# Kernel optimization log

Hardware: AMD Instinct MI355X
Metric: run time of the kernel (lower is better)

## Reference

```python
import jax, jax.numpy as jnp
import numpy as np

N, B, C, H = 1024, 4, 256, 8
D = C // H


def _make_boxes(k):
    u = jax.random.uniform(k, (N, 4), dtype=jnp.float32)
    x1 = u[:, 0] * 500.0
    y1 = u[:, 1] * 500.0
    x2 = x1 + u[:, 2] * 200.0 + 1.0
    y2 = y1 + u[:, 3] * 200.0 + 1.0
    return jnp.stack([x1, y1, x2, y2], axis=1)


def setup_inputs() -> dict:
    rng = jax.random.key(0)
    ks = jax.random.split(rng, 10)
    s = 1.0 / np.sqrt(C)
    return {
        "query": jax.random.normal(ks[0], (N, B, C), dtype=jnp.float32),
        "key": jax.random.normal(ks[1], (N, B, C), dtype=jnp.float32),
        "value": jax.random.normal(ks[2], (N, B, C), dtype=jnp.float32),
        "q_boxes": _make_boxes(ks[3]),
        "k_boxes": _make_boxes(ks[4]),
        "Wq": jax.random.normal(ks[5], (C, C), dtype=jnp.float32) * s,
        "Wk": jax.random.normal(ks[6], (C, C), dtype=jnp.float32) * s,
        "Wv": jax.random.normal(ks[7], (C, C), dtype=jnp.float32) * s,
        "pos_w": jax.random.normal(ks[8], (H, 64), dtype=jnp.float32) * 0.125,
        "pos_b": jax.random.normal(ks[9], (H,), dtype=jnp.float32) * 0.01,
    }


def _position_bias(qb, kb, pos_w, pos_b):
    # extract_position_matrix: boxes are x1y1x2y2, shapes [N,4]
    cx, cy = 0.5 * (qb[:, 0] + qb[:, 2]), 0.5 * (qb[:, 1] + qb[:, 3])
    w, h = qb[:, 2] - qb[:, 0] + 1.0, qb[:, 3] - qb[:, 1] + 1.0
    cxr, cyr = 0.5 * (kb[:, 0] + kb[:, 2]), 0.5 * (kb[:, 1] + kb[:, 3])
    wr, hr = kb[:, 2] - kb[:, 0] + 1.0, kb[:, 3] - kb[:, 1] + 1.0
    dx = jnp.log(jnp.abs((cx[:, None] - cxr[None, :]) / w[:, None]) + 1e-3)
    dy = jnp.log(jnp.abs((cy[:, None] - cyr[None, :]) / h[:, None]) + 1e-3)
    dw = jnp.log(w[:, None] / wr[None, :])
    dh = jnp.log(h[:, None] / hr[None, :])
    pm = jnp.stack([dx, dy, dw, dh], axis=2)  # [N, N, 4]
    # extract_position_embedding: feat_dim=64 -> 8 sinusoid frequencies
    dim_mat = 1000.0 ** (jnp.arange(8, dtype=jnp.float32) * (8.0 / 64.0))
    div = pm[..., None] * 100.0 / dim_mat  # [N, N, 4, 8]
    emb = jnp.concatenate([jnp.sin(div), jnp.cos(div)], axis=3)
    emb = emb.reshape(pm.shape[0], pm.shape[1], 64)  # [N, N, 64]
    # 1x1 Conv2d(64 -> H) over the [64, N, N] map == channel matmul
    pe = jnp.einsum('nmc,hc->hnm', emb, pos_w) + pos_b[:, None, None]
    return jnp.log(jax.nn.relu(pe) + 1e-6)  # [H, N, N]


def reference(query, key, value, q_boxes, k_boxes, Wq, Wk, Wv, pos_w, pos_b):
    n, b, c = query.shape
    d = c // H

    def proj(x, W):
        # nn.Linear (no bias): x @ W.T ; reshape (N,B,H,D) -> (B,H,N,D)
        return (x @ W.T).reshape(n, b, H, d).transpose(1, 2, 0, 3)

    q = proj(query, Wq)
    k = proj(key, Wk)
    v = proj(value, Wv)
    # cosine normalization of q and k
    q = q / jnp.linalg.norm(q, axis=-1, keepdims=True)
    k = k / jnp.linalg.norm(k, axis=-1, keepdims=True)
    attn_reg = jax.nn.softmax(jnp.einsum('bhnd,bhmd->bhnm', q, k), axis=-1)
    # log of relu'd conv position embedding added AFTER softmax (as in source)
    attn = attn_reg + _position_bias(q_boxes, k_boxes, pos_w, pos_b)[None]
    out = jnp.einsum('bhnm,bhmd->bhnd', attn, v)  # [B,H,N,D]
    out = out.transpose(0, 2, 1, 3).reshape(b, n, c).transpose(1, 0, 2)  # [N,B,C]
    return (out, attn)
```

## Files before the change

kernel.cpp:

```cpp
#include <hip/hip_runtime.h>
#include <hip/hip_bf16.h>
#include <math.h>

#define PN 1024
#define PB 4
#define PC 256
#define PH 8
#define PD 32

typedef __attribute__((ext_vector_type(8))) short bf16x8;
typedef __attribute__((ext_vector_type(4))) float f32x4;

__device__ __forceinline__ unsigned short f2b(float f) {
    unsigned int u = __builtin_bit_cast(unsigned int, f);
    unsigned int r = (u + 0x7fffu + ((u >> 16) & 1u)) >> 16;
    return (unsigned short)r;
}
__device__ __forceinline__ float b2f(unsigned short u) {
    return __builtin_bit_cast(float, ((unsigned int)u) << 16);
}
__device__ __forceinline__ bf16x8 ldf8(const float* p) {
    float4 u0 = ((const float4*)p)[0];
    float4 u1 = ((const float4*)p)[1];
    bf16x8 r;
    r[0] = (short)f2b(u0.x); r[1] = (short)f2b(u0.y);
    r[2] = (short)f2b(u0.z); r[3] = (short)f2b(u0.w);
    r[4] = (short)f2b(u1.x); r[5] = (short)f2b(u1.y);
    r[6] = (short)f2b(u1.z); r[7] = (short)f2b(u1.w);
    return r;
}

__global__ __launch_bounds__(256) void proj_mfma(
    const float* __restrict__ xq, const float* __restrict__ xk, const float* __restrict__ xv,
    const float* __restrict__ wq, const float* __restrict__ wk, const float* __restrict__ wv,
    unsigned short* __restrict__ qb, unsigned short* __restrict__ kb, unsigned short* __restrict__ vt)
{
    const int z = blockIdx.z;
    const float* X = (z == 0) ? xq : (z == 1) ? xk : xv;
    const float* W = (z == 0) ? wq : (z == 1) ? wk : wv;

    const int row0 = blockIdx.x * 64, col0 = blockIdx.y * 64;
    const int tid = threadIdx.x;
    const int w = tid >> 6, l = tid & 63;
    const int l15 = l & 15, lg = l >> 4;
    const int wm = w >> 1, wn = w & 1;

    f32x4 acc[2][2];
    #pragma unroll
    for (int a = 0; a < 2; a++)
        #pragma unroll
        for (int b = 0; b < 2; b++) acc[a][b] = (f32x4){0.f, 0.f, 0.f, 0.f};

    #pragma unroll
    for (int ks = 0; ks < 8; ks++) {
        int koff = ks * 32 + lg * 8;
        bf16x8 a0 = ldf8(X + (size_t)(row0 + wm * 32 + l15) * 256 + koff);
        bf16x8 a1 = ldf8(X + (size_t)(row0 + wm * 32 + 16 + l15) * 256 + koff);
        bf16x8 b0 = ldf8(W + (size_t)(col0 + wn * 32 + l15) * 256 + koff);
        bf16x8 b1 = ldf8(W + (size_t)(col0 + wn * 32 + 16 + l15) * 256 + koff);
        acc[0][0] = __builtin_amdgcn_mfma_f32_16x16x32_bf16(a0, b0, acc[0][0], 0, 0, 0);
        acc[0][1] = __builtin_amdgcn_mfma_f32_16x16x32_bf16(a0, b1, acc[0][1], 0, 0, 0);
        acc[1][0] = __builtin_amdgcn_mfma_f32_16x16x32_bf16(a1, b0, acc[1][0], 0, 0, 0);
        acc[1][1] = __builtin_amdgcn_mfma_f32_16x16x32_bf16(a1, b1, acc[1][1], 0, 0, 0);
    }

    if (z < 2) {
        #pragma unroll
        for (int as = 0; as < 2; as++) {
            #pragma unroll
            for (int r = 0; r < 4; r++) {
                float ss = acc[as][0][r] * acc[as][0][r] + acc[as][1][r] * acc[as][1][r];
                ss += __shfl_xor(ss, 1);
                ss += __shfl_xor(ss, 2);
                ss += __shfl_xor(ss, 4);
                ss += __shfl_xor(ss, 8);
                float inv = rsqrtf(ss);
                acc[as][0][r] *= inv;
                acc[as][1][r] *= inv;
            }
        }
    }

    #pragma unroll
    for (int as = 0; as < 2; as++) {
        #pragma unroll
        for (int bs = 0; bs < 2; bs++) {
            #pragma unroll
            for (int r = 0; r < 4; r++) {
                int Xrow = row0 + wm * 32 + as * 16 + lg * 4 + r;
                int c = col0 + wn * 32 + bs * 16 + l15;
                int n = Xrow >> 2, bb = Xrow & 3, hh = c >> 5, dd = c & 31;
                unsigned short val = f2b(acc[as][bs][r]);
                if (z == 0)      qb[((size_t)((bb * 8 + hh) * 1024 + n)) * 32 + dd] = val;
                else if (z == 1) kb[((size_t)((bb * 8 + hh) * 1024 + n)) * 32 + dd] = val;
                else             vt[((size_t)((bb * 8 + hh) * 32 + dd)) * 1024 + n] = val;
            }
        }
    }
}

__global__ __launch_bounds__(256) void bias_kernel(
    const float* __restrict__ qbx, const float* __restrict__ kbx,
    const float* __restrict__ pw, const float* __restrict__ pb,
    unsigned short* __restrict__ biasb)
{
    __shared__ float4 pwS[128];
    __shared__ float pbS[8];
    int tid = threadIdx.x;
    if (tid < 128) pwS[tid] = ((const float4*)pw)[tid];
    if (tid < 8) pbS[tid] = pb[tid];
    __syncthreads();

    int idx = blockIdx.x * 256 + tid;
    int n = idx >> 10, m = idx & 1023;

    float4 qx = ((const float4*)qbx)[n];
    float4 kx = ((const float4*)kbx)[m];

    float cx = 0.5f * (qx.x + qx.z), cy = 0.5f * (qx.y + qx.w);
    float w  = qx.z - qx.x + 1.0f,   hh = qx.w - qx.y + 1.0f;
    float cxr = 0.5f * (kx.x + kx.z), cyr = 0.5f * (kx.y + kx.w);
    float wr  = kx.z - kx.x + 1.0f,   hr  = kx.w - kx.y + 1.0f;

    float pm[4];
    pm[0] = __logf(fabsf((cx - cxr) / w) + 1e-3f);
    pm[1] = __logf(fabsf((cy - cyr) / hh) + 1e-3f);
    pm[2] = __logf(w / wr);
    pm[3] = __logf(hh / hr);

    const float inv[8] = {100.f, 42.1696503f, 17.7827941f, 7.49894209f,
                          3.16227766f, 1.33352143f, 0.562341325f, 0.237137371f};

    float emb[64];
    #pragma unroll
    for (int p = 0; p < 4; p++) {
        #pragma unroll
        for (int i = 0; i < 8; i++) {
            float a = pm[p] * inv[i];
            emb[p * 16 + i]     = __sinf(a);
            emb[p * 16 + 8 + i] = __cosf(a);
        }
    }

    #pragma unroll
    for (int h = 0; h < PH; h++) {
        float acc = pbS[h];
        #pragma unroll
        for (int c4 = 0; c4 < 16; c4++) {
            float4 w4 = pwS[h * 16 + c4];
            acc += emb[c4 * 4 + 0] * w4.x + emb[c4 * 4 + 1] * w4.y
                 + emb[c4 * 4 + 2] * w4.z + emb[c4 * 4 + 3] * w4.w;
        }
        float bv = __logf(fmaxf(acc, 0.f) + 1e-6f);
        biasb[((size_t)(h * 1024 + n)) * 1024 + m] = f2b(bv);
    }
}

#define SBS 1032

__global__ __launch_bounds__(512, 4) void attn_kernel(
    const unsigned short* __restrict__ qb, const unsigned short* __restrict__ kb,
    const unsigned short* __restrict__ vt, const unsigned short* __restrict__ biasb,
    float* __restrict__ out, float* __restrict__ attn_out)
{
    __shared__ unsigned short Sb[16][SBS];
    __shared__ float part[8][16][17];

    const int bh = blockIdx.y;
    const int b = bh >> 3, h = bh & 7;
    const int n0 = blockIdx.x * 16;
    const int tid = threadIdx.x;
    const int w = tid >> 6, l = tid & 63;
    const int l15 = l & 15, lg = l >> 4;

    {
        const int qrow = n0 + l15;
        bf16x8 aq = *(const bf16x8*)(qb + ((size_t)(bh << 10) + qrow) * 32 + lg * 8);
        #pragma unroll
        for (int t = 0; t < 8; ++t) {
            int key = w * 128 + t * 16 + l15;
            bf16x8 bk = *(const bf16x8*)(kb + ((size_t)(bh << 10) + key) * 32 + lg * 8);
            f32x4 acc = (f32x4){0.f, 0.f, 0.f, 0.f};
            acc = __builtin_amdgcn_mfma_f32_16x16x32_bf16(aq, bk, acc, 0, 0, 0);
            #pragma unroll
            for (int r = 0; r < 4; ++r)
                Sb[lg * 4 + r][key] = f2b(acc[r]);
        }
    }
    __syncthreads();

    {
        #pragma unroll
        for (int rr = 0; rr < 2; ++rr) {
            int r = w * 2 + rr;
            float s[16];
            #pragma unroll
            for (int i = 0; i < 16; ++i) s[i] = b2f(Sb[r][l + 64 * i]);
            float mx = s[0];
            #pragma unroll
            for (int i = 1; i < 16; ++i) mx = fmaxf(mx, s[i]);
            #pragma unroll
            for (int off = 32; off > 0; off >>= 1) mx = fmaxf(mx, __shfl_xor(mx, off));
            float e[16], sum = 0.f;
            #pragma unroll
            for (int i = 0; i < 16; ++i) { e[i] = __expf(s[i] - mx); sum += e[i]; }
            #pragma unroll
            for (int off = 32; off > 0; off >>= 1) sum += __shfl_xor(sum, off);
            float invs = 1.f / sum;

            const unsigned short* brow = biasb + ((size_t)(h * 1024 + n0 + r)) * 1024;
            float* arow = attn_out + ((size_t)(bh * 1024 + n0 + r)) * 1024;
            #pragma unroll
            for (int i = 0; i < 16; ++i) {
                int m = l + 64 * i;
                float a = e[i] * invs + b2f(brow[m]);
                arow[m] = a;
                Sb[r][m] = f2b(a);
            }
        }
    }
    __syncthreads();

    {
        const int ds = w >> 2, kh = w & 3;
        f32x4 acc = (f32x4){0.f, 0.f, 0.f, 0.f};
        const unsigned short* vrow = vt + ((size_t)(bh * 32 + ds * 16 + l15) << 10);
        const unsigned short* srow = &Sb[l15][0];
        #pragma unroll
        for (int st = 0; st < 8; ++st) {
            int m0 = kh * 256 + st * 32 + lg * 8;
            bf16x8 ap = *(const bf16x8*)(srow + m0);
            bf16x8 bv = *(const bf16x8*)(vrow + m0);
            acc = __builtin_amdgcn_mfma_f32_16x16x32_bf16(ap, bv, acc, 0, 0, 0);
        }
        #pragma unroll
        for (int r = 0; r < 4; ++r) part[w][lg * 4 + r][l15] = acc[r];
    }
    __syncthreads();

    {
        int q = tid >> 5, d = tid & 31;
        int ds = d >> 4, d15 = d & 15;
        float v = part[ds * 4 + 0][q][d15] + part[ds * 4 + 1][q][d15]
                + part[ds * 4 + 2][q][d15] + part[ds * 4 + 3][q][d15];
        out[((size_t)(n0 + q) * PB + b) * PC + h * PD + d] = v;
    }
}

extern "C" void kernel_launch(void* const* d_in, const int* in_sizes, int n_in,
                              void* d_out, int out_size, void* d_ws, size_t ws_size,
                              hipStream_t stream)
{
    const float* query   = (const float*)d_in[0];
    const float* key     = (const float*)d_in[1];
    const float* value   = (const float*)d_in[2];
    const float* q_boxes = (const float*)d_in[3];
    const float* k_boxes = (const float*)d_in[4];
    const float* Wq      = (const float*)d_in[5];
    const float* Wk      = (const float*)d_in[6];
    const float* Wv      = (const float*)d_in[7];
    const float* pos_w   = (const float*)d_in[8];
    const float* pos_b   = (const float*)d_in[9];

    unsigned short* u = (unsigned short*)d_ws;
    unsigned short* qbf  = u;
    unsigned short* kbf  = qbf + 1048576;
    unsigned short* vtb  = kbf + 1048576;
    unsigned short* bias = vtb + 1048576;

    float* out  = (float*)d_out;
    float* attn = out + (size_t)PN * PB * PC;

    proj_mfma<<<dim3(64, 4, 3), 256, 0, stream>>>(query, key, value, Wq, Wk, Wv,
                                                  qbf, kbf, vtb);
    bias_kernel<<<dim3(4096), 256, 0, stream>>>(q_boxes, k_boxes, pos_w, pos_b, bias);
    attn_kernel<<<dim3(64, 32), 512, 0, stream>>>(qbf, kbf, vtb, bias, out, attn);
}
```

Measured before the change: 233.2 us.

## Compute position-bias channel matmul with split-bf16 MFMA in bias kernel

The bias kernel is reorganised so that each wave handles one query box against 16 key boxes. The lanes split the 64 sinusoid channels between them. The 64->8 channel projection is done with bf16 MFMA instructions, using a hi/lo split of both the embedding and the weights to keep near-fp32 accuracy. This replaces 512 scalar FMAs per pair and the LDS weight staging. In exchange it adds conversion work and per-lane global weight loads, and only half the lanes write outputs, in 4-element runs. The launch grid becomes 2D (16 x 1024).

```diff
diff --git a/kernel.cpp b/kernel.cpp
--- a/kernel.cpp
+++ b/kernel.cpp
@@ -104,55 +104,76 @@
     const float* __restrict__ pw, const float* __restrict__ pb,
     unsigned short* __restrict__ biasb)
 {
-    __shared__ float4 pwS[128];
-    __shared__ float pbS[8];
-    int tid = threadIdx.x;
-    if (tid < 128) pwS[tid] = ((const float4*)pw)[tid];
-    if (tid < 8) pbS[tid] = pb[tid];
-    __syncthreads();
-
-    int idx = blockIdx.x * 256 + tid;
-    int n = idx >> 10, m = idx & 1023;
+    const int tid = threadIdx.x;
+    const int w = tid >> 6, l = tid & 63;
+    const int l15 = l & 15, lg = l >> 4;
+    const int n = blockIdx.y;
+    const int mbase = blockIdx.x * 64 + w * 16;
+    const int m = mbase + l15;
+    const int lgh = lg >> 1, lgl = lg & 1;
 
     float4 qx = ((const float4*)qbx)[n];
     float4 kx = ((const float4*)kbx)[m];
-
     float cx = 0.5f * (qx.x + qx.z), cy = 0.5f * (qx.y + qx.w);
-    float w  = qx.z - qx.x + 1.0f,   hh = qx.w - qx.y + 1.0f;
+    float bw = qx.z - qx.x + 1.0f,   bh = qx.w - qx.y + 1.0f;
     float cxr = 0.5f * (kx.x + kx.z), cyr = 0.5f * (kx.y + kx.w);
     float wr  = kx.z - kx.x + 1.0f,   hr  = kx.w - kx.y + 1.0f;
 
     float pm[4];
-    pm[0] = __logf(fabsf((cx - cxr) / w) + 1e-3f);
-    pm[1] = __logf(fabsf((cy - cyr) / hh) + 1e-3f);
-    pm[2] = __logf(w / wr);
-    pm[3] = __logf(hh / hr);
-
-    const float inv[8] = {100.f, 42.1696503f, 17.7827941f, 7.49894209f,
-                          3.16227766f, 1.33352143f, 0.562341325f, 0.237137371f};
-
-    float emb[64];
-    #pragma unroll
-    for (int p = 0; p < 4; p++) {
-        #pragma unroll
-        for (int i = 0; i < 8; i++) {
-            float a = pm[p] * inv[i];
-            emb[p * 16 + i]     = __sinf(a);
-            emb[p * 16 + 8 + i] = __cosf(a);
-        }
-    }
-
-    #pragma unroll
-    for (int h = 0; h < PH; h++) {
-        float acc = pbS[h];
-        #pragma unroll
-        for (int c4 = 0; c4 < 16; c4++) {
-            float4 w4 = pwS[h * 16 + c4];
-            acc += emb[c4 * 4 + 0] * w4.x + emb[c4 * 4 + 1] * w4.y
-                 + emb[c4 * 4 + 2] * w4.z + emb[c4 * 4 + 3] * w4.w;
-        }
-        float bv = __logf(fmaxf(acc, 0.f) + 1e-6f);
-        biasb[((size_t)(h * 1024 + n)) * 1024 + m] = f2b(bv);
+    pm[0] = __logf(fabsf((cx - cxr) / bw) + 1e-3f);
+    pm[1] = __logf(fabsf((cy - cyr) / bh) + 1e-3f);
+    pm[2] = __logf(bw / wr);
+    pm[3] = __logf(bh / hr);
+
+    const float f_lo[4] = {100.f, 42.1696503f, 17.7827941f, 7.49894209f};
+    const float f_hi[4] = {3.16227766f, 1.33352143f, 0.562341325f, 0.237137371f};
+
+    bf16x8 ahi[2], alo[2], bhi[2], blo[2];
+    const int h = l15;
+    #pragma unroll
+    for (int s = 0; s < 2; s++) {
+        float pmv = lgh ? pm[s * 2 + 1] : pm[s * 2];
+        int p = s * 2 + lgh;
+        #pragma unroll
+        for (int c = 0; c < 4; c++) {
+            float fi = lgl ? f_hi[c] : f_lo[c];
+            float a = pmv * fi;
+            float sv = __sinf(a), cv = __cosf(a);
+            unsigned short sh = f2b(sv), ch = f2b(cv);
+            unsigned short sl = f2b(sv - b2f(sh)), cl = f2b(cv - b2f(ch));
+            ahi[s][2 * c] = (short)sh; ahi[s][2 * c + 1] = (short)ch;
+            alo[s][2 * c] = (short)sl; alo[s][2 * c + 1] = (short)cl;
+
+            float wsv = 0.f, wcv = 0.f;
+            if (h < 8) {
+                int i = lgl * 4 + c;
+                wsv = pw[h * 64 + p * 16 + i];
+                wcv = pw[h * 64 + p * 16 + 8 + i];
+            }
+            unsigned short wsh = f2b(wsv), wch = f2b(wcv);
+            unsigned short wsl = f2b(wsv - b2f(wsh)), wcl = f2b(wcv - b2f(wch));
+            bhi[s][2 * c] = (short)wsh; bhi[s][2 * c + 1] = (short)wch;
+            blo[s][2 * c] = (short)wsl; blo[s][2 * c + 1] = (short)wcl;
+        }
+    }
+
+    f32x4 acc = (f32x4){0.f, 0.f, 0.f, 0.f};
+    #pragma unroll
+    for (int s = 0; s < 2; s++) {
+        acc = __builtin_amdgcn_mfma_f32_16x16x32_bf16(ahi[s], bhi[s], acc, 0, 0, 0);
+        acc = __builtin_amdgcn_mfma_f32_16x16x32_bf16(alo[s], bhi[s], acc, 0, 0, 0);
+        acc = __builtin_amdgcn_mfma_f32_16x16x32_bf16(ahi[s], blo[s], acc, 0, 0, 0);
+    }
+
+    if (l15 < 8) {
+        float pbv = pb[l15];
+        #pragma unroll
+        for (int r = 0; r < 4; r++) {
+            int mg = mbase + lg * 4 + r;
+            float v = acc[r] + pbv;
+            float bv = __logf(fmaxf(v, 0.f) + 1e-6f);
+            biasb[((size_t)(l15 * 1024 + n)) * 1024 + mg] = f2b(bv);
+        }
     }
 }
 
@@ -273,6 +294,6 @@
 
     proj_mfma<<<dim3(64, 4, 3), 256, 0, stream>>>(query, key, value, Wq, Wk, Wv,
                                                   qbf, kbf, vtb);
-    bias_kernel<<<dim3(4096), 256, 0, stream>>>(q_boxes, k_boxes, pos_w, pos_b, bias);
+    bias_kernel<<<dim3(16, 1024), 256, 0, stream>>>(q_boxes, k_boxes, pos_w, pos_b, bias);
     attn_kernel<<<dim3(64, 32), 512, 0, stream>>>(qbf, kbf, vtb, bias, out, attn);
 }
```

Result: slower. 299.5 us (+28.4%).
